# Kernel optimization log

Measured on AMD Instinct MI355X. Metric: run time of the kernel, lower is better.

Reference implementation:

```python
import jax, jax.numpy as jnp
import numpy as np

B, N, M = 16, 4096, 1024
C_IN, C_SKIP, C_OUT = 256, 128, 256
K = 3
BN_EPS = 1e-5


def setup_inputs() -> dict:
    key = jax.random.key(0)
    ks = jax.random.split(key, 6)
    s1 = (6.0 / (C_IN + C_SKIP + C_OUT)) ** 0.5  # xavier-uniform bound, ~scale
    s2 = (6.0 / (2 * C_OUT)) ** 0.5
    return {
        "points": jax.random.normal(ks[0], (B, 3, N), jnp.float32),
        "point_features": jax.random.normal(ks[1], (B, C_SKIP, N), jnp.float32),
        "centroids": jax.random.normal(ks[2], (B, 3, M), jnp.float32),
        "centroid_features": jax.random.normal(ks[3], (B, C_IN, M), jnp.float32),
        "W1": jax.random.uniform(ks[4], (C_OUT, C_IN + C_SKIP), jnp.float32, -s1, s1),
        "b1": jnp.zeros((C_OUT,), jnp.float32),
        "gamma": jnp.ones((C_OUT,), jnp.float32),
        "beta": jnp.zeros((C_OUT,), jnp.float32),
        "W2": jax.random.uniform(ks[5], (C_OUT, C_OUT), jnp.float32, -s2, s2),
        "b2": jnp.zeros((C_OUT,), jnp.float32),
    }


def _knn_interpolate(x, pos_x, pos_y):
    # x: [B,M,C], pos_x: [B,M,3], pos_y: [B,N,3]. torch_geometric knn_interpolate, k=3.
    d2 = (jnp.sum(pos_y * pos_y, -1)[:, :, None]
          + jnp.sum(pos_x * pos_x, -1)[:, None, :]
          - 2.0 * jnp.einsum('bnd,bmd->bnm', pos_y, pos_x))  # [B,N,M]
    neg_vals, idx = jax.lax.top_k(-d2, K)                    # k smallest distances
    w = 1.0 / jnp.maximum(-neg_vals, 1e-16)                  # inverse-squared-distance weights
    # original computes indices/weights under torch.no_grad()
    idx = jax.lax.stop_gradient(idx)
    w = jax.lax.stop_gradient(w)
    xk = jax.vmap(lambda xb, ib: xb[ib])(x, idx)             # [B,N,K,C]
    return jnp.einsum('bnkc,bnk->bnc', xk, w) / jnp.sum(w, -1, keepdims=True)


def reference(points, point_features, centroids, centroid_features,
              W1, b1, gamma, beta, W2, b2):
    # Faithful to the original torch .reshape/.view calls on channel-first layout
    pos_y = points.reshape(-1, 3).reshape(B, N, 3)
    pos_x = centroids.reshape(-1, 3).reshape(B, M, 3)
    x = centroid_features.reshape(-1, C_IN).reshape(B, M, C_IN)
    interp = _knn_interpolate(x, pos_x, pos_y)               # [B,N,C_IN]
    interp = interp.reshape(-1, C_IN).reshape(B, C_IN, N)    # faithful .view(B, C, -1)
    h = jnp.concatenate([point_features, interp], axis=1)    # [B, C_SKIP+C_IN, N]
    # Conv1d(kernel=1) -> channel GEMM
    h = jnp.einsum('oc,bcn->bon', W1, h) + b1[None, :, None]
    # BatchNorm1d, training mode (biased batch var), eps=1e-5
    mean = jnp.mean(h, axis=(0, 2), keepdims=True)
    var = jnp.var(h, axis=(0, 2), keepdims=True)
    h = (h - mean) * jax.lax.rsqrt(var + BN_EPS) * gamma[None, :, None] + beta[None, :, None]
    h = jax.nn.relu(h)
    return jnp.einsum('oc,bcn->bon', W2, h) + b2[None, :, None]
```

## Files before the change

### kernel.cpp

```cpp
#include <hip/hip_runtime.h>

#define BB   16
#define NN   4096
#define MM   1024
#define CIN  256
#define CSK  128
#define COUT 256
#define KCH  384
#define NP   65536
#define NSEG2 512
#define NCHUNK 8
#define MCH  (MM / NCHUNK)
#define CVB  32

typedef __attribute__((ext_vector_type(8))) short bf16x8;
typedef __attribute__((ext_vector_type(4))) float f32x4;
typedef __attribute__((ext_vector_type(8))) unsigned short ushort8v;
typedef __attribute__((ext_vector_type(4))) unsigned short ushort4v;

static __device__ __forceinline__ unsigned short f2bf(float f) {
    unsigned u = __builtin_bit_cast(unsigned, f);
    u += 0x7fffu + ((u >> 16) & 1u);
    return (unsigned short)(u >> 16);
}
static __device__ __forceinline__ float bf2f(unsigned short h) {
    unsigned u = ((unsigned)h) << 16;
    return __builtin_bit_cast(float, u);
}

__global__ __launch_bounds__(256) void prep_kernel(
    const float* __restrict__ pf, unsigned short* __restrict__ HbT,
    const float* __restrict__ W1, const float* __restrict__ W2,
    unsigned short* __restrict__ W1b, unsigned short* __restrict__ W2b,
    const float* __restrict__ cen, float4* __restrict__ cen4)
{
    __shared__ float ls[64][129];
    int blk = blockIdx.x;
    int t = threadIdx.x;
    if (blk >= 1664) {
        int i = (blk - 1664) * 256 + t;
        const float* cb = cen + (size_t)i * 3;
        float x = cb[0], y = cb[1], z = cb[2];
        cen4[i] = make_float4(x, y, z, x*x + y*y + z*z);
        return;
    }
    if (blk >= 1024) {
        int i = (blk - 1024) * 256 + t;
        if (i < COUT * KCH) W1b[i] = f2bf(W1[i]);
        else {
            int j = i - COUT * KCH;
            if (j < COUT * COUT) W2b[j] = f2bf(W2[j]);
        }
        return;
    }
    int b = blk >> 6, n0 = (blk & 63) * 64;
    const float* src = pf + (size_t)b * CSK * NN;
    #pragma unroll
    for (int i = 0; i < 32; ++i) {
        int id = t + i * 256;
        int c = id >> 6, nn = id & 63;
        ls[nn][c] = src[(size_t)c * NN + n0 + nn];
    }
    __syncthreads();
    int row = t & 63, ch = (t >> 6) * 32;
    unsigned short* dst = HbT + ((size_t)b * NN + n0 + row) * KCH + ch;
    #pragma unroll
    for (int g = 0; g < 4; ++g) {
        ushort8v w;
        #pragma unroll
        for (int j = 0; j < 8; ++j) w[j] = f2bf(ls[row][ch + g*8 + j]);
        *(ushort8v*)&dst[g*8] = w;
    }
}

__global__ __launch_bounds__(256) void knn_part_kernel(
    const float* __restrict__ pts, const float4* __restrict__ cen4,
    float* __restrict__ pdist, int* __restrict__ pidx)
{
    int p0    = blockIdx.x * 256;
    int chunk = blockIdx.y;
    int b     = p0 >> 12;
    int m0    = chunk * MCH;
    const float4* cb4 = cen4 + (size_t)b * MM + m0;

    int p = p0 + threadIdx.x;
    int n = p & (NN - 1);
    const float* pb = pts + (size_t)b * 3 * NN;
    float px = pb[3*n], py = pb[3*n+1], pz = pb[3*n+2];
    float pw = px*px + py*py + pz*pz;

    float d0 = 1e30f, d1 = 1e30f, d2v = 1e30f;
    int   i0 = 0, i1 = 0, i2 = 0;
    #pragma unroll 16
    for (int m = 0; m < MCH; ++m) {
        float4 c = cb4[m];
        float dot = px*c.x + py*c.y + pz*c.z;
        float d = (pw + c.w) - 2.0f * dot;
        bool c0 = d < d0, c1 = d < d1, c2 = d < d2v;
        int ni2 = c1 ? i1 : (c2 ? m : i2);
        int ni1 = c0 ? i0 : (c1 ? m : i1);
        int ni0 = c0 ? m  : i0;
        float nd1 = __builtin_amdgcn_fmed3f(d, d0, d1);
        float nd2 = __builtin_amdgcn_fmed3f(d, d1, d2v);
        d0 = fminf(d0, d);
        d1 = nd1; d2v = nd2;
        i0 = ni0; i1 = ni1; i2 = ni2;
    }
    int base = (p * NCHUNK + chunk) * 3;
    pdist[base] = d0;      pdist[base+1] = d1;      pdist[base+2] = d2v;
    pidx[base]  = m0 + i0; pidx[base+1]  = m0 + i1; pidx[base+2]  = m0 + i2;
}

__global__ __launch_bounds__(256) void interp_kernel(
    const float* __restrict__ cf, const float* __restrict__ pdist,
    const int* __restrict__ pidx, unsigned short* __restrict__ HbT)
{
    __shared__ int   li[CVB][3];
    __shared__ float lw[CVB][3];
    __shared__ unsigned short tile[CVB][258];
    int bh = blockIdx.x;
    int b = bh >> 4, hi = bh & 15;
    int ch = blockIdx.y;
    int t = threadIdx.x;
    if (t < CVB) {
        int P = b * NN + (ch * CVB + t) * 16 + hi;
        float d0 = 1e30f, d1 = 1e30f, d2v = 1e30f;
        int   i0 = 0, i1 = 0, i2 = 0;
        int base = P * NCHUNK * 3;
        #pragma unroll
        for (int c = 0; c < NCHUNK * 3; ++c) {
            float d = pdist[base + c];
            int   i = pidx[base + c];
            bool c2 = d < d2v, c1 = d < d1, c0 = d < d0;
            d2v = c1 ? d1 : (c2 ? d : d2v);
            i2  = c1 ? i1 : (c2 ? i : i2);
            d1  = c0 ? d0 : (c1 ? d : d1);
            i1  = c0 ? i0 : (c1 ? i : i1);
            d0  = c0 ? d  : d0;
            i0  = c0 ? i  : i0;
        }
        float w0 = 1.0f / fmaxf(d0,  1e-16f);
        float w1 = 1.0f / fmaxf(d1,  1e-16f);
        float w2 = 1.0f / fmaxf(d2v, 1e-16f);
        float inv = 1.0f / (w0 + w1 + w2);
        li[t][0] = i0;     li[t][1] = i1;     li[t][2] = i2;
        lw[t][0] = w0*inv; lw[t][1] = w1*inv; lw[t][2] = w2*inv;
    }
    __syncthreads();
    const float* cfb = cf + (size_t)b * MM * CIN;
    #pragma unroll 4
    for (int cv = 0; cv < CVB; ++cv) {
        float v = lw[cv][0] * cfb[(size_t)li[cv][0] * CIN + t]
                + lw[cv][1] * cfb[(size_t)li[cv][1] * CIN + t]
                + lw[cv][2] * cfb[(size_t)li[cv][2] * CIN + t];
        tile[cv][t] = f2bf(v);
    }
    __syncthreads();
    size_t dstbase = ((size_t)b * NN + hi * 256 + t) * KCH + CSK + ch * CVB;
    #pragma unroll
    for (int g = 0; g < CVB / 8; ++g) {
        ushort8v w;
        #pragma unroll
        for (int j = 0; j < 8; ++j) w[j] = tile[g*8 + j][t];
        *(ushort8v*)&HbT[dstbase + g*8] = w;
    }
}

__global__ __launch_bounds__(256) void gemm1_kernel(
    const unsigned short* __restrict__ HbT, const unsigned short* __restrict__ W1b,
    const float* __restrict__ b1, unsigned short* __restrict__ h1T,
    float* __restrict__ psum, float* __restrict__ psq)
{
    __shared__ __align__(16) unsigned short As[128][40];
    __shared__ __align__(16) unsigned short Bs[128][40];
    int pp0 = blockIdx.x * 128;
    int o0  = blockIdx.y * 128;
    int t = threadIdx.x;
    int wid = t >> 6, lane = t & 63;
    int wr = wid >> 1, wc = wid & 1;
    int lr = lane & 15, lk = lane >> 4;

    int rowi[2], qi[2];
    ushort8v ra[2], rb[2];
    #pragma unroll
    for (int i = 0; i < 2; ++i) { int id = t + i*256; rowi[i] = id >> 2; qi[i] = id & 3; }
    #pragma unroll
    for (int i = 0; i < 2; ++i) {
        ra[i] = *(const ushort8v*)&W1b[(size_t)(o0 + rowi[i]) * KCH + qi[i]*8];
        rb[i] = *(const ushort8v*)&HbT[(size_t)(pp0 + rowi[i]) * KCH + qi[i]*8];
    }

    f32x4 acc[4][4] = {};

    for (int c0 = 0; c0 < KCH; c0 += 32) {
        #pragma unroll
        for (int i = 0; i < 2; ++i) {
            *(ushort8v*)&As[rowi[i]][qi[i]*8] = ra[i];
            *(ushort8v*)&Bs[rowi[i]][qi[i]*8] = rb[i];
        }
        __syncthreads();
        int cn = (c0 + 32 < KCH) ? c0 + 32 : c0;
        #pragma unroll
        for (int i = 0; i < 2; ++i) {
            ra[i] = *(const ushort8v*)&W1b[(size_t)(o0 + rowi[i]) * KCH + cn + qi[i]*8];
            rb[i] = *(const ushort8v*)&HbT[(size_t)(pp0 + rowi[i]) * KCH + cn + qi[i]*8];
        }
        bf16x8 af[4], bfr[4];
        #pragma unroll
        for (int m = 0; m < 4; ++m) af[m] = *(const bf16x8*)&As[wr*64 + m*16 + lr][lk*8];
        #pragma unroll
        for (int n = 0; n < 4; ++n) bfr[n] = *(const bf16x8*)&Bs[wc*64 + n*16 + lr][lk*8];
        #pragma unroll
        for (int m = 0; m < 4; ++m)
            #pragma unroll
            for (int n = 0; n < 4; ++n)
                acc[m][n] = __builtin_amdgcn_mfma_f32_16x16x32_bf16(af[m], bfr[n], acc[m][n], 0, 0, 0);
        __syncthreads();
    }
    float sprt[4][4] = {{0.f}}, qprt[4][4] = {{0.f}};
    #pragma unroll
    for (int n = 0; n < 4; ++n) {
        int p = pp0 + wc*64 + n*16 + lr;
        #pragma unroll
        for (int m = 0; m < 4; ++m) {
            int o = o0 + wr*64 + m*16 + lk*4;
            f32x4 v = acc[m][n];
            ushort4v w;
            #pragma unroll
            for (int j = 0; j < 4; ++j) {
                float f = v[j] + b1[o + j];
                w[j] = f2bf(f);
                float r = bf2f(w[j]);
                sprt[m][j] += r;
                qprt[m][j] = fmaf(r, r, qprt[m][j]);
            }
            *(ushort4v*)&h1T[(size_t)p * COUT + o] = w;
        }
    }
    #pragma unroll
    for (int m = 0; m < 4; ++m)
        #pragma unroll
        for (int j = 0; j < 4; ++j) {
            float s = sprt[m][j], q = qprt[m][j];
            #pragma unroll
            for (int off = 1; off < 16; off <<= 1) {
                s += __shfl_xor(s, off, 64);
                q += __shfl_xor(q, off, 64);
            }
            sprt[m][j] = s; qprt[m][j] = q;
        }
    float* sred = (float*)As;
    float* qred = sred + 256;
    if (lr == 0) {
        #pragma unroll
        for (int m = 0; m < 4; ++m)
            #pragma unroll
            for (int j = 0; j < 4; ++j) {
                int ol = wr*64 + m*16 + lk*4 + j;
                sred[wc*128 + ol] = sprt[m][j];
                qred[wc*128 + ol] = qprt[m][j];
            }
    }
    __syncthreads();
    if (t < 128) {
        float S = sred[t] + sred[128 + t];
        float Q = qred[t] + qred[128 + t];
        psum[(size_t)(o0 + t) * NSEG2 + blockIdx.x] = S;
        psq [(size_t)(o0 + t) * NSEG2 + blockIdx.x] = Q;
    }
}

__global__ __launch_bounds__(256) void bnfin_kernel(
    const float* __restrict__ psum, const float* __restrict__ psq,
    const float* __restrict__ gamma, const float* __restrict__ beta,
    float* __restrict__ bnscale, float* __restrict__ bnshift)
{
    __shared__ float rs[256], rq[256];
    int o = blockIdx.x, t = threadIdx.x;
    rs[t] = psum[(size_t)o * NSEG2 + t] + psum[(size_t)o * NSEG2 + 256 + t];
    rq[t] = psq [(size_t)o * NSEG2 + t] + psq [(size_t)o * NSEG2 + 256 + t];
    __syncthreads();
    for (int off = 128; off > 0; off >>= 1) {
        if (t < off) { rs[t] += rs[t + off]; rq[t] += rq[t + off]; }
        __syncthreads();
    }
    if (t == 0) {
        float mean = rs[0] * (1.0f / NP);
        float var  = rq[0] * (1.0f / NP) - mean * mean;
        float sc = gamma[o] * rsqrtf(var + 1e-5f);
        bnscale[o] = sc;
        bnshift[o] = fmaf(-mean, sc, beta[o]);
    }
}

__global__ __launch_bounds__(256) void gemm2_kernel(
    const unsigned short* __restrict__ h1T, const unsigned short* __restrict__ W2b,
    const float* __restrict__ b2, const float* __restrict__ bnscale,
    const float* __restrict__ bnshift, float* __restrict__ out)
{
    __shared__ union {
        struct {
            __align__(16) unsigned short As[128][40];
            __align__(16) unsigned short Bs[128][40];
        } s;
        float eps[64][132];
    } u;
    __shared__ float scs[COUT], shs[COUT];
    int pp0 = blockIdx.x * 128;
    int o0  = blockIdx.y * 128;
    int t = threadIdx.x;
    scs[t] = bnscale[t]; shs[t] = bnshift[t];
    int wid = t >> 6, lane = t & 63;
    int wr = wid >> 1, wc = wid & 1;
    int lr = lane & 15, lk = lane >> 4;

    int rowi[2], qi[2];
    ushort8v ra[2], rb[2];
    #pragma unroll
    for (int i = 0; i < 2; ++i) { int id = t + i*256; rowi[i] = id >> 2; qi[i] = id & 3; }
    #pragma unroll
    for (int i = 0; i < 2; ++i) {
        ra[i] = *(const ushort8v*)&W2b[(size_t)(o0 + rowi[i]) * COUT + qi[i]*8];
        rb[i] = *(const ushort8v*)&h1T[(size_t)(pp0 + rowi[i]) * COUT + qi[i]*8];
    }
    f32x4 acc[4][4] = {};
    __syncthreads();

    for (int c0 = 0; c0 < COUT; c0 += 32) {
        #pragma unroll
        for (int i = 0; i < 2; ++i) {
            *(ushort8v*)&u.s.As[rowi[i]][qi[i]*8] = ra[i];
            ushort8v bv;
            #pragma unroll
            for (int j = 0; j < 8; ++j) {
                float f = fmaf(bf2f(rb[i][j]), scs[c0 + qi[i]*8 + j], shs[c0 + qi[i]*8 + j]);
                bv[j] = f2bf(fmaxf(f, 0.0f));
            }
            *(ushort8v*)&u.s.Bs[rowi[i]][qi[i]*8] = bv;
        }
        __syncthreads();
        int cn = (c0 + 32 < COUT) ? c0 + 32 : c0;
        #pragma unroll
        for (int i = 0; i < 2; ++i) {
            ra[i] = *(const ushort8v*)&W2b[(size_t)(o0 + rowi[i]) * COUT + cn + qi[i]*8];
            rb[i] = *(const ushort8v*)&h1T[(size_t)(pp0 + rowi[i]) * COUT + cn + qi[i]*8];
        }
        bf16x8 af[4], bfr[4];
        #pragma unroll
        for (int m = 0; m < 4; ++m) af[m] = *(const bf16x8*)&u.s.As[wr*64 + m*16 + lr][lk*8];
        #pragma unroll
        for (int n = 0; n < 4; ++n) bfr[n] = *(const bf16x8*)&u.s.Bs[wc*64 + n*16 + lr][lk*8];
        #pragma unroll
        for (int m = 0; m < 4; ++m)
            #pragma unroll
            for (int n = 0; n < 4; ++n)
                acc[m][n] = __builtin_amdgcn_mfma_f32_16x16x32_bf16(af[m], bfr[n], acc[m][n], 0, 0, 0);
        __syncthreads();
    }
    int b  = pp0 >> 12;
    int n0 = pp0 & (NN - 1);
    float b2v[4][4];
    #pragma unroll
    for (int m = 0; m < 4; ++m)
        #pragma unroll
        for (int j = 0; j < 4; ++j)
            b2v[m][j] = b2[o0 + wr*64 + m*16 + lk*4 + j];
    #pragma unroll
    for (int ow = 0; ow < 2; ++ow) {
        if (wr == ow) {
            #pragma unroll
            for (int m = 0; m < 4; ++m)
                #pragma unroll
                for (int n = 0; n < 4; ++n) {
                    f32x4 v = acc[m][n];
                    int pl = wc*64 + n*16 + lr;
                    #pragma unroll
                    for (int j = 0; j < 4; ++j)
                        u.eps[m*16 + lk*4 + j][pl] = v[j] + b2v[m][j];
                }
        }
        __syncthreads();
        #pragma unroll
        for (int i = 0; i < 8; ++i) {
            int r  = (t >> 5) + i * 8;
            int c4 = (t & 31) * 4;
            float4 v = *(const float4*)&u.eps[r][c4];
            *(float4*)&out[((size_t)(b * COUT + o0 + ow*64 + r)) * NN + n0 + c4] = v;
        }
        __syncthreads();
    }
}

extern "C" void kernel_launch(void* const* d_in, const int* in_sizes, int n_in,
                              void* d_out, int out_size, void* d_ws, size_t ws_size,
                              hipStream_t stream)
{
    const float* pts   = (const float*)d_in[0];
    const float* pf    = (const float*)d_in[1];
    const float* cen   = (const float*)d_in[2];
    const float* cf    = (const float*)d_in[3];
    const float* W1    = (const float*)d_in[4];
    const float* b1    = (const float*)d_in[5];
    const float* gamma = (const float*)d_in[6];
    const float* beta  = (const float*)d_in[7];
    const float* W2    = (const float*)d_in[8];
    const float* b2    = (const float*)d_in[9];
    float* out = (float*)d_out;

    char* ws = (char*)d_ws;
    size_t off = 0;
    unsigned short* HbT = (unsigned short*)(ws + off); off += (size_t)NP * KCH * 2;
    unsigned short* h1T = (unsigned short*)(ws + off); off += (size_t)NP * COUT * 2;
    unsigned short* W1b = (unsigned short*)(ws + off); off += (size_t)COUT * KCH * 2;
    unsigned short* W2b = (unsigned short*)(ws + off); off += (size_t)COUT * COUT * 2;
    float* pdist   = (float*)(ws + off); off += (size_t)NP * NCHUNK * 3 * sizeof(float);
    int*   pidx    = (int*)(ws + off);   off += (size_t)NP * NCHUNK * 3 * sizeof(int);
    float4* cen4   = (float4*)(ws + off); off += (size_t)BB * MM * sizeof(float4);
    float* psum    = (float*)(ws + off); off += (size_t)COUT * NSEG2 * sizeof(float);
    float* psq     = (float*)(ws + off); off += (size_t)COUT * NSEG2 * sizeof(float);
    float* bnscale = (float*)(ws + off); off += 1024;
    float* bnshift = (float*)(ws + off); off += 1024;
    (void)ws_size; (void)in_sizes; (void)n_in; (void)out_size;

    hipLaunchKernelGGL(prep_kernel,     dim3(1728),              dim3(256), 0, stream,
                       pf, HbT, W1, W2, W1b, W2b, cen, cen4);
    hipLaunchKernelGGL(knn_part_kernel, dim3(NP / 256, NCHUNK),  dim3(256), 0, stream,
                       pts, cen4, pdist, pidx);
    hipLaunchKernelGGL(interp_kernel,   dim3(256, 8),            dim3(256), 0, stream,
                       cf, pdist, pidx, HbT);
    hipLaunchKernelGGL(gemm1_kernel,    dim3(NP / 128, 2),       dim3(256), 0, stream,
                       HbT, W1b, b1, h1T, psum, psq);
    hipLaunchKernelGGL(bnfin_kernel,    dim3(COUT),              dim3(256), 0, stream,
                       psum, psq, gamma, beta, bnscale, bnshift);
    hipLaunchKernelGGL(gemm2_kernel,    dim3(NP / 128, 2),       dim3(256), 0, stream,
                       h1T, W2b, b2, bnscale, bnshift, out);
}
```

Before: 151.4 us.

## Merge prep and kNN into one kernel, bf16 centroid features, staged gemm1 stores

Folds the prep and kNN-partial kernels into a single launch. The kNN blocks build their centroid float4 cache in shared memory, and extra block ranges convert centroid features to bf16 and transpose the skip features. interp now gathers bf16 centroid features, which halves gather bytes, and remaps blocks so each XCD handles a fixed pair of batches for L2 locality. gemm1 stages its output tile through shared memory for coalesced 16-byte stores and hoists bias loads. The changes add an extra rounding of interpolation inputs to bf16 and an extra conversion pass over the centroid features.

```diff
diff --git a/kernel.cpp b/kernel.cpp
--- a/kernel.cpp
+++ b/kernel.cpp
@@ -28,99 +28,117 @@
     return __builtin_bit_cast(float, u);
 }
 
-__global__ __launch_bounds__(256) void prep_kernel(
+__global__ __launch_bounds__(256) void megak_kernel(
+    const float* __restrict__ pts, const float* __restrict__ cen,
+    float* __restrict__ pdist, int* __restrict__ pidx,
+    const float* __restrict__ cf, unsigned short* __restrict__ cfb,
     const float* __restrict__ pf, unsigned short* __restrict__ HbT,
     const float* __restrict__ W1, const float* __restrict__ W2,
-    unsigned short* __restrict__ W1b, unsigned short* __restrict__ W2b,
-    const float* __restrict__ cen, float4* __restrict__ cen4)
-{
-    __shared__ float ls[64][129];
+    unsigned short* __restrict__ W1b, unsigned short* __restrict__ W2b)
+{
+    __shared__ union { float4 sc[MCH]; float ls[64][65]; } su;
     int blk = blockIdx.x;
     int t = threadIdx.x;
-    if (blk >= 1664) {
-        int i = (blk - 1664) * 256 + t;
-        const float* cb = cen + (size_t)i * 3;
-        float x = cb[0], y = cb[1], z = cb[2];
-        cen4[i] = make_float4(x, y, z, x*x + y*y + z*z);
+
+    if (blk < 2048) {
+        int p0    = (blk >> 3) * 256;
+        int chunk = blk & 7;
+        int b     = p0 >> 12;
+        int m0    = chunk * MCH;
+        const float* cb = cen + (size_t)b * 3 * MM + 3 * m0;
+        if (t < MCH) {
+            float x = cb[3*t], y = cb[3*t+1], z = cb[3*t+2];
+            su.sc[t] = make_float4(x, y, z, x*x + y*y + z*z);
+        }
+        __syncthreads();
+
+        int p = p0 + t;
+        int n = p & (NN - 1);
+        const float* pb = pts + (size_t)b * 3 * NN;
+        float px = pb[3*n], py = pb[3*n+1], pz = pb[3*n+2];
+        float pw = px*px + py*py + pz*pz;
+
+        float d0 = 1e30f, d1 = 1e30f, d2v = 1e30f;
+        int   i0 = 0, i1 = 0, i2 = 0;
+        #pragma unroll 16
+        for (int m = 0; m < MCH; ++m) {
+            float4 c = su.sc[m];
+            float dot = px*c.x + py*c.y + pz*c.z;
+            float d = (pw + c.w) - 2.0f * dot;
+            bool c0 = d < d0, c1 = d < d1, c2 = d < d2v;
+            int ni2 = c1 ? i1 : (c2 ? m : i2);
+            int ni1 = c0 ? i0 : (c1 ? m : i1);
+            int ni0 = c0 ? m  : i0;
+            float nd1 = __builtin_amdgcn_fmed3f(d, d0, d1);
+            float nd2 = __builtin_amdgcn_fmed3f(d, d1, d2v);
+            d0 = fminf(d0, d);
+            d1 = nd1; d2v = nd2;
+            i0 = ni0; i1 = ni1; i2 = ni2;
+        }
+        int base = (p * NCHUNK + chunk) * 3;
+        pdist[base] = d0;      pdist[base+1] = d1;      pdist[base+2] = d2v;
+        pidx[base]  = m0 + i0; pidx[base+1]  = m0 + i1; pidx[base+2]  = m0 + i2;
         return;
     }
-    if (blk >= 1024) {
-        int i = (blk - 1024) * 256 + t;
+    if (blk < 4096) {
+        int g = blk - 2048;
+        size_t e8 = ((size_t)g * 256 + t) * 8;
+        const float4* cf4 = (const float4*)(cf + e8);
+        float4 a = cf4[0], b4 = cf4[1];
+        ushort8v w;
+        w[0]=f2bf(a.x); w[1]=f2bf(a.y); w[2]=f2bf(a.z); w[3]=f2bf(a.w);
+        w[4]=f2bf(b4.x); w[5]=f2bf(b4.y); w[6]=f2bf(b4.z); w[7]=f2bf(b4.w);
+        *(ushort8v*)&cfb[e8] = w;
+        return;
+    }
+    if (blk < 6144) {
+        int g = blk - 4096;
+        int b = g >> 7;
+        int r = g & 127;
+        int n0 = (r >> 1) * 64;
+        int c0 = (r & 1) * 64;
+        const float* src = pf + (size_t)b * CSK * NN;
+        #pragma unroll
+        for (int i = 0; i < 16; ++i) {
+            int id = t + i * 256;
+            int cc = id >> 6, nn = id & 63;
+            su.ls[nn][cc] = src[(size_t)(c0 + cc) * NN + n0 + nn];
+        }
+        __syncthreads();
+        int row = t & 63, ch0 = (t >> 6) * 16;
+        unsigned short* dst = HbT + ((size_t)b * NN + n0 + row) * KCH + c0 + ch0;
+        #pragma unroll
+        for (int g2 = 0; g2 < 2; ++g2) {
+            ushort8v w;
+            #pragma unroll
+            for (int j = 0; j < 8; ++j) w[j] = f2bf(su.ls[row][ch0 + g2*8 + j]);
+            *(ushort8v*)&dst[g2*8] = w;
+        }
+        return;
+    }
+    {
+        int i = (blk - 6144) * 256 + t;
         if (i < COUT * KCH) W1b[i] = f2bf(W1[i]);
         else {
             int j = i - COUT * KCH;
             if (j < COUT * COUT) W2b[j] = f2bf(W2[j]);
         }
-        return;
-    }
-    int b = blk >> 6, n0 = (blk & 63) * 64;
-    const float* src = pf + (size_t)b * CSK * NN;
-    #pragma unroll
-    for (int i = 0; i < 32; ++i) {
-        int id = t + i * 256;
-        int c = id >> 6, nn = id & 63;
-        ls[nn][c] = src[(size_t)c * NN + n0 + nn];
-    }
-    __syncthreads();
-    int row = t & 63, ch = (t >> 6) * 32;
-    unsigned short* dst = HbT + ((size_t)b * NN + n0 + row) * KCH + ch;
-    #pragma unroll
-    for (int g = 0; g < 4; ++g) {
-        ushort8v w;
-        #pragma unroll
-        for (int j = 0; j < 8; ++j) w[j] = f2bf(ls[row][ch + g*8 + j]);
-        *(ushort8v*)&dst[g*8] = w;
-    }
-}
-
-__global__ __launch_bounds__(256) void knn_part_kernel(
-    const float* __restrict__ pts, const float4* __restrict__ cen4,
-    float* __restrict__ pdist, int* __restrict__ pidx)
-{
-    int p0    = blockIdx.x * 256;
-    int chunk = blockIdx.y;
-    int b     = p0 >> 12;
-    int m0    = chunk * MCH;
-    const float4* cb4 = cen4 + (size_t)b * MM + m0;
-
-    int p = p0 + threadIdx.x;
-    int n = p & (NN - 1);
-    const float* pb = pts + (size_t)b * 3 * NN;
-    float px = pb[3*n], py = pb[3*n+1], pz = pb[3*n+2];
-    float pw = px*px + py*py + pz*pz;
-
-    float d0 = 1e30f, d1 = 1e30f, d2v = 1e30f;
-    int   i0 = 0, i1 = 0, i2 = 0;
-    #pragma unroll 16
-    for (int m = 0; m < MCH; ++m) {
-        float4 c = cb4[m];
-        float dot = px*c.x + py*c.y + pz*c.z;
-        float d = (pw + c.w) - 2.0f * dot;
-        bool c0 = d < d0, c1 = d < d1, c2 = d < d2v;
-        int ni2 = c1 ? i1 : (c2 ? m : i2);
-        int ni1 = c0 ? i0 : (c1 ? m : i1);
-        int ni0 = c0 ? m  : i0;
-        float nd1 = __builtin_amdgcn_fmed3f(d, d0, d1);
-        float nd2 = __builtin_amdgcn_fmed3f(d, d1, d2v);
-        d0 = fminf(d0, d);
-        d1 = nd1; d2v = nd2;
-        i0 = ni0; i1 = ni1; i2 = ni2;
-    }
-    int base = (p * NCHUNK + chunk) * 3;
-    pdist[base] = d0;      pdist[base+1] = d1;      pdist[base+2] = d2v;
-    pidx[base]  = m0 + i0; pidx[base+1]  = m0 + i1; pidx[base+2]  = m0 + i2;
+    }
 }
 
 __global__ __launch_bounds__(256) void interp_kernel(
-    const float* __restrict__ cf, const float* __restrict__ pdist,
+    const unsigned short* __restrict__ cfb, const float* __restrict__ pdist,
     const int* __restrict__ pidx, unsigned short* __restrict__ HbT)
 {
     __shared__ int   li[CVB][3];
     __shared__ float lw[CVB][3];
     __shared__ unsigned short tile[CVB][258];
-    int bh = blockIdx.x;
-    int b = bh >> 4, hi = bh & 15;
-    int ch = blockIdx.y;
+    int xcd = blockIdx.x & 7;
+    int j   = blockIdx.x >> 3;
+    int b   = xcd * 2 + (j >> 7);
+    int rem = j & 127;
+    int hi  = rem >> 3;
+    int ch  = rem & 7;
     int t = threadIdx.x;
     if (t < CVB) {
         int P = b * NN + (ch * CVB + t) * 16 + hi;
@@ -147,12 +165,12 @@
         lw[t][0] = w0*inv; lw[t][1] = w1*inv; lw[t][2] = w2*inv;
     }
     __syncthreads();
-    const float* cfb = cf + (size_t)b * MM * CIN;
+    const unsigned short* cfbb = cfb + (size_t)b * MM * CIN;
     #pragma unroll 4
     for (int cv = 0; cv < CVB; ++cv) {
-        float v = lw[cv][0] * cfb[(size_t)li[cv][0] * CIN + t]
-                + lw[cv][1] * cfb[(size_t)li[cv][1] * CIN + t]
-                + lw[cv][2] * cfb[(size_t)li[cv][2] * CIN + t];
+        float v = lw[cv][0] * bf2f(cfbb[(size_t)li[cv][0] * CIN + t])
+                + lw[cv][1] * bf2f(cfbb[(size_t)li[cv][1] * CIN + t])
+                + lw[cv][2] * bf2f(cfbb[(size_t)li[cv][2] * CIN + t]);
         tile[cv][t] = f2bf(v);
     }
     __syncthreads();
@@ -161,7 +179,7 @@
     for (int g = 0; g < CVB / 8; ++g) {
         ushort8v w;
         #pragma unroll
-        for (int j = 0; j < 8; ++j) w[j] = tile[g*8 + j][t];
+        for (int j2 = 0; j2 < 8; ++j2) w[j2] = tile[g*8 + j2][t];
         *(ushort8v*)&HbT[dstbase + g*8] = w;
     }
 }
@@ -171,8 +189,16 @@
     const float* __restrict__ b1, unsigned short* __restrict__ h1T,
     float* __restrict__ psum, float* __restrict__ psq)
 {
-    __shared__ __align__(16) unsigned short As[128][40];
-    __shared__ __align__(16) unsigned short Bs[128][40];
+    __shared__ union {
+        struct {
+            __align__(16) unsigned short As[128][40];
+            __align__(16) unsigned short Bs[128][40];
+        } s;
+        struct {
+            __align__(16) unsigned short eps[64][136];
+            float red[512];
+        } e;
+    } u;
     int pp0 = blockIdx.x * 128;
     int o0  = blockIdx.y * 128;
     int t = threadIdx.x;
@@ -195,8 +221,8 @@
     for (int c0 = 0; c0 < KCH; c0 += 32) {
         #pragma unroll
         for (int i = 0; i < 2; ++i) {
-            *(ushort8v*)&As[rowi[i]][qi[i]*8] = ra[i];
-            *(ushort8v*)&Bs[rowi[i]][qi[i]*8] = rb[i];
+            *(ushort8v*)&u.s.As[rowi[i]][qi[i]*8] = ra[i];
+            *(ushort8v*)&u.s.Bs[rowi[i]][qi[i]*8] = rb[i];
         }
         __syncthreads();
         int cn = (c0 + 32 < KCH) ? c0 + 32 : c0;
@@ -207,9 +233,9 @@
         }
         bf16x8 af[4], bfr[4];
         #pragma unroll
-        for (int m = 0; m < 4; ++m) af[m] = *(const bf16x8*)&As[wr*64 + m*16 + lr][lk*8];
-        #pragma unroll
-        for (int n = 0; n < 4; ++n) bfr[n] = *(const bf16x8*)&Bs[wc*64 + n*16 + lr][lk*8];
+        for (int m = 0; m < 4; ++m) af[m] = *(const bf16x8*)&u.s.As[wr*64 + m*16 + lr][lk*8];
+        #pragma unroll
+        for (int n = 0; n < 4; ++n) bfr[n] = *(const bf16x8*)&u.s.Bs[wc*64 + n*16 + lr][lk*8];
         #pragma unroll
         for (int m = 0; m < 4; ++m)
             #pragma unroll
@@ -217,25 +243,46 @@
                 acc[m][n] = __builtin_amdgcn_mfma_f32_16x16x32_bf16(af[m], bfr[n], acc[m][n], 0, 0, 0);
         __syncthreads();
     }
+    float bb[4][4];
+    #pragma unroll
+    for (int m = 0; m < 4; ++m)
+        #pragma unroll
+        for (int j = 0; j < 4; ++j)
+            bb[m][j] = b1[o0 + wr*64 + m*16 + lk*4 + j];
     float sprt[4][4] = {{0.f}}, qprt[4][4] = {{0.f}};
     #pragma unroll
-    for (int n = 0; n < 4; ++n) {
-        int p = pp0 + wc*64 + n*16 + lr;
-        #pragma unroll
-        for (int m = 0; m < 4; ++m) {
-            int o = o0 + wr*64 + m*16 + lk*4;
-            f32x4 v = acc[m][n];
-            ushort4v w;
-            #pragma unroll
-            for (int j = 0; j < 4; ++j) {
-                float f = v[j] + b1[o + j];
-                w[j] = f2bf(f);
-                float r = bf2f(w[j]);
-                sprt[m][j] += r;
-                qprt[m][j] = fmaf(r, r, qprt[m][j]);
+    for (int pw = 0; pw < 2; ++pw) {
+        if (wc == pw) {
+            #pragma unroll
+            for (int n = 0; n < 4; ++n) {
+                int r = n*16 + lr;
+                #pragma unroll
+                for (int m = 0; m < 4; ++m) {
+                    f32x4 v = acc[m][n];
+                    ushort4v w;
+                    #pragma unroll
+                    for (int j = 0; j < 4; ++j) {
+                        float f = v[j] + bb[m][j];
+                        w[j] = f2bf(f);
+                        float rr = bf2f(w[j]);
+                        sprt[m][j] += rr;
+                        qprt[m][j] = fmaf(rr, rr, qprt[m][j]);
+                    }
+                    *(ushort4v*)&u.e.eps[r][wr*64 + m*16 + lk*4] = w;
+                }
             }
-            *(ushort4v*)&h1T[(size_t)p * COUT + o] = w;
-        }
+        }
+        __syncthreads();
+        {
+            int r = t >> 2, seg = t & 3;
+            size_t gbase = ((size_t)(pp0 + pw*64 + r)) * COUT + o0 + seg * 32;
+            #pragma unroll
+            for (int k = 0; k < 4; ++k) {
+                ushort8v vv = *(const ushort8v*)&u.e.eps[r][seg*32 + k*8];
+                *(ushort8v*)&h1T[gbase + k*8] = vv;
+            }
+        }
+        __syncthreads();
     }
     #pragma unroll
     for (int m = 0; m < 4; ++m)
@@ -249,22 +296,20 @@
             }
             sprt[m][j] = s; qprt[m][j] = q;
         }
-    float* sred = (float*)As;
-    float* qred = sred + 256;
     if (lr == 0) {
         #pragma unroll
         for (int m = 0; m < 4; ++m)
             #pragma unroll
             for (int j = 0; j < 4; ++j) {
                 int ol = wr*64 + m*16 + lk*4 + j;
-                sred[wc*128 + ol] = sprt[m][j];
-                qred[wc*128 + ol] = qprt[m][j];
+                u.e.red[wc*128 + ol]       = sprt[m][j];
+                u.e.red[256 + wc*128 + ol] = qprt[m][j];
             }
     }
     __syncthreads();
     if (t < 128) {
-        float S = sred[t] + sred[128 + t];
-        float Q = qred[t] + qred[128 + t];
+        float S = u.e.red[t] + u.e.red[128 + t];
+        float Q = u.e.red[256 + t] + u.e.red[384 + t];
         psum[(size_t)(o0 + t) * NSEG2 + blockIdx.x] = S;
         psq [(size_t)(o0 + t) * NSEG2 + blockIdx.x] = Q;
     }
@@ -413,25 +458,23 @@
     unsigned short* h1T = (unsigned short*)(ws + off); off += (size_t)NP * COUT * 2;
     unsigned short* W1b = (unsigned short*)(ws + off); off += (size_t)COUT * KCH * 2;
     unsigned short* W2b = (unsigned short*)(ws + off); off += (size_t)COUT * COUT * 2;
+    unsigned short* cfb = (unsigned short*)(ws + off); off += (size_t)BB * MM * CIN * 2;
     float* pdist   = (float*)(ws + off); off += (size_t)NP * NCHUNK * 3 * sizeof(float);
     int*   pidx    = (int*)(ws + off);   off += (size_t)NP * NCHUNK * 3 * sizeof(int);
-    float4* cen4   = (float4*)(ws + off); off += (size_t)BB * MM * sizeof(float4);
     float* psum    = (float*)(ws + off); off += (size_t)COUT * NSEG2 * sizeof(float);
     float* psq     = (float*)(ws + off); off += (size_t)COUT * NSEG2 * sizeof(float);
     float* bnscale = (float*)(ws + off); off += 1024;
     float* bnshift = (float*)(ws + off); off += 1024;
     (void)ws_size; (void)in_sizes; (void)n_in; (void)out_size;
 
-    hipLaunchKernelGGL(prep_kernel,     dim3(1728),              dim3(256), 0, stream,
-                       pf, HbT, W1, W2, W1b, W2b, cen, cen4);
-    hipLaunchKernelGGL(knn_part_kernel, dim3(NP / 256, NCHUNK),  dim3(256), 0, stream,
-                       pts, cen4, pdist, pidx);
-    hipLaunchKernelGGL(interp_kernel,   dim3(256, 8),            dim3(256), 0, stream,
-                       cf, pdist, pidx, HbT);
-    hipLaunchKernelGGL(gemm1_kernel,    dim3(NP / 128, 2),       dim3(256), 0, stream,
+    hipLaunchKernelGGL(megak_kernel,  dim3(6784),         dim3(256), 0, stream,
+                       pts, cen, pdist, pidx, cf, cfb, pf, HbT, W1, W2, W1b, W2b);
+    hipLaunchKernelGGL(interp_kernel, dim3(2048),         dim3(256), 0, stream,
+                       cfb, pdist, pidx, HbT);
+    hipLaunchKernelGGL(gemm1_kernel,  dim3(NP / 128, 2),  dim3(256), 0, stream,
                        HbT, W1b, b1, h1T, psum, psq);
-    hipLaunchKernelGGL(bnfin_kernel,    dim3(COUT),              dim3(256), 0, stream,
+    hipLaunchKernelGGL(bnfin_kernel,  dim3(COUT),         dim3(256), 0, stream,
                        psum, psq, gamma, beta, bnscale, bnshift);
-    hipLaunchKernelGGL(gemm2_kernel,    dim3(NP / 128, 2),       dim3(256), 0, stream,
+    hipLaunchKernelGGL(gemm2_kernel,  dim3(NP / 128, 2),  dim3(256), 0, stream,
                        h1T, W2b, b2, bnscale, bnshift, out);
 }
```

After: 134.2 us. 1.13x faster.
